# Kernel optimization log

Hardware: AMD Instinct MI355X
Metric: run time of the kernel (lower is better)

The kernel has to match this reference:

```python
import jax, jax.numpy as jnp
import numpy as np

B, S, D = 4, 1568, 1024
H = 16
HD = D // H  # 64


def setup_inputs() -> dict:
    key = jax.random.key(0)
    ks = jax.random.split(key, 9)
    scale = 0.02
    return {
        "hidden_states": jax.random.normal(ks[0], (B, S, D), dtype=jnp.float32),
        "Wq": jax.random.normal(ks[1], (D, D), dtype=jnp.float32) * scale,
        "bq": jnp.zeros((D,), dtype=jnp.float32),
        "Wk": jax.random.normal(ks[2], (D, D), dtype=jnp.float32) * scale,
        "bk": jnp.zeros((D,), dtype=jnp.float32),
        "Wv": jax.random.normal(ks[3], (D, D), dtype=jnp.float32) * scale,
        "bv": jnp.zeros((D,), dtype=jnp.float32),
        "Wp": jax.random.normal(ks[4], (D, D), dtype=jnp.float32) * scale,
        "bp": jnp.zeros((D,), dtype=jnp.float32),
    }


def reference(hidden_states, Wq, bq, Wk, bk, Wv, bv, Wp, bp):
    x = hidden_states  # [B, S, D]
    # Linear projections (torch Linear: x @ W.T + b)
    q = x @ Wq.T + bq
    k = x @ Wk.T + bk
    v = x @ Wv.T + bv
    # split heads: [B, H, S, HD]
    def heads(t):
        return t.reshape(B, S, H, HD).transpose(0, 2, 1, 3)
    q, k, v = heads(q), heads(k), heads(v)
    scale = 1.0 / jnp.sqrt(jnp.asarray(HD, dtype=q.dtype))
    scores = jnp.einsum('bhqd,bhkd->bhqk', q, k) * scale  # [B,H,S,S]
    probs = jax.nn.softmax(scores, axis=-1)
    ctx = jnp.einsum('bhqk,bhkd->bhqd', probs, v)  # [B,H,S,HD]
    ctx = ctx.transpose(0, 2, 1, 3).reshape(B, S, D)
    out = ctx @ Wp.T + bp
    return out
```

## Files before the change

kernel.cpp:

```cpp
#include <hip/hip_runtime.h>
#include <stdint.h>

#define SEQ 1568
#define SEQV 1600
#define DIM 1024
#define NB 4
#define NH 16
#define HD 64

typedef unsigned short u16;
typedef __bf16 bf16x8 __attribute__((ext_vector_type(8)));
typedef float f32x4 __attribute__((ext_vector_type(4)));

#define QSCALE 0.18033688011112042f

#define PSTR 72

__device__ __forceinline__ void load_lds16(const u16* g, u16* s) {
  __builtin_amdgcn_global_load_lds((__attribute__((address_space(1))) void*)g,
                                   (__attribute__((address_space(3))) void*)s,
                                   16, 0, 0);
}

__global__ __launch_bounds__(256) void cvt_all(
    const float* __restrict__ x,  const float* __restrict__ wq,
    const float* __restrict__ wk, const float* __restrict__ wv,
    const float* __restrict__ wp,
    u16* __restrict__ xb, u16* __restrict__ wqb, u16* __restrict__ wkb,
    u16* __restrict__ wvb, u16* __restrict__ wpb) {
  int i = blockIdx.x * 256 + threadIdx.x;
  const float* src; u16* dst; int off;
  if (i < 1605632)      { src = x;  dst = xb;  off = i; }
  else if (i < 1867776) { src = wq; dst = wqb; off = i - 1605632; }
  else if (i < 2129920) { src = wk; dst = wkb; off = i - 1867776; }
  else if (i < 2392064) { src = wv; dst = wvb; off = i - 2129920; }
  else                  { src = wp; dst = wpb; off = i - 2392064; }
  float4 v = ((const float4*)src)[off];
  union { unsigned long long u; __bf16 h[4]; } o;
  o.h[0] = (__bf16)v.x; o.h[1] = (__bf16)v.y;
  o.h[2] = (__bf16)v.z; o.h[3] = (__bf16)v.w;
  ((unsigned long long*)dst)[off] = o.u;
}

__global__ __launch_bounds__(256) void gemm_qkv(
    const u16* __restrict__ xb,
    const u16* __restrict__ wq, const u16* __restrict__ wk, const u16* __restrict__ wv,
    const float* __restrict__ bq, const float* __restrict__ bk, const float* __restrict__ bv,
    u16* __restrict__ qo, u16* __restrict__ ko, u16* __restrict__ vto) {
  const int z = blockIdx.z;
  const u16* W = (z == 0) ? wq : (z == 1) ? wk : wv;
  const float* bias = (z == 0) ? bq : (z == 1) ? bk : bv;

  __shared__ __align__(16) u16 sA[128 * 32];
  __shared__ __align__(16) u16 sB[128 * 32];

  const int tid = threadIdx.x;
  const int wave = tid >> 6;
  const int lane = tid & 63;
  const int l15 = lane & 15;
  const int quad = lane >> 4;
  const int bi = blockIdx.y / 13;
  const int st = blockIdx.y % 13;
  const int bn = blockIdx.x * 128;
  const int wm = (wave >> 1) * 64;
  const int wn = (wave & 1) * 64;

  const int sr = lane >> 2;
  const int sc = (lane & 3) * 8;
  const int r0 = wave * 32;

  f32x4 acc[4][4] = {};

  for (int k0 = 0; k0 < DIM; k0 += 32) {
    __syncthreads();
    {
      int sr1 = st * 128 + r0 + sr;       if (sr1 >= SEQ) sr1 = SEQ - 1;
      int sr2 = st * 128 + r0 + 16 + sr;  if (sr2 >= SEQ) sr2 = SEQ - 1;
      load_lds16(xb + (size_t)(bi * SEQ + sr1) * DIM + k0 + sc, &sA[r0 * 32]);
      load_lds16(xb + (size_t)(bi * SEQ + sr2) * DIM + k0 + sc, &sA[(r0 + 16) * 32]);
      const u16* gB = W + (size_t)(bn + r0 + sr) * DIM + k0 + sc;
      load_lds16(gB, &sB[r0 * 32]);
      load_lds16(gB + 16 * DIM, &sB[(r0 + 16) * 32]);
    }
    __syncthreads();

    bf16x8 a[4], b[4];
#pragma unroll
    for (int mt = 0; mt < 4; mt++)
      a[mt] = *(const bf16x8*)&sA[(wm + mt * 16 + l15) * 32 + quad * 8];
#pragma unroll
    for (int nt = 0; nt < 4; nt++)
      b[nt] = *(const bf16x8*)&sB[(wn + nt * 16 + l15) * 32 + quad * 8];
#pragma unroll
    for (int mt = 0; mt < 4; mt++)
#pragma unroll
      for (int nt = 0; nt < 4; nt++)
        acc[mt][nt] = __builtin_amdgcn_mfma_f32_16x16x32_bf16(a[mt], b[nt], acc[mt][nt], 0, 0, 0);
  }

#pragma unroll
  for (int nt = 0; nt < 4; nt++) {
    const int n = bn + wn + nt * 16 + l15;
    const float bia = bias[n];
    const int h = n >> 6, d = n & 63;
#pragma unroll
    for (int mt = 0; mt < 4; mt++) {
      const int sbase = st * 128 + wm + mt * 16 + quad * 4;
#pragma unroll
      for (int r = 0; r < 4; r++) {
        const int s = sbase + r;
        if (s < SEQ) {
          float val = acc[mt][nt][r] + bia;
          if (z == 0) val *= QSCALE;
          const __bf16 o = (__bf16)val;
          if (z == 0)
            *(__bf16*)&qo[(((size_t)(bi * NH + h)) * SEQ + s) * HD + d] = o;
          else if (z == 1)
            *(__bf16*)&ko[(((size_t)(bi * NH + h)) * SEQ + s) * HD + d] = o;
          else
            *(__bf16*)&vto[(((size_t)(bi * NH + h)) * HD + d) * SEQV + s] = o;
        }
      }
    }
  }
}

__global__ __launch_bounds__(256, 4) void attn(
    const u16* __restrict__ q, const u16* __restrict__ k,
    const u16* __restrict__ vt, u16* __restrict__ ctx) {
  const int bh = blockIdx.y;
  const int qt = blockIdx.x;
  const int tid = threadIdx.x;
  const int wave = tid >> 6, lane = tid & 63, l15 = lane & 15, quad = lane >> 4;

  __shared__ __align__(16) u16 sK[64 * 64];
  __shared__ __align__(16) u16 sV[64 * 64];
  __shared__ __align__(16) u16 sP[4][32 * PSTR];

  const u16* qh = q + (size_t)bh * (SEQ * HD);
  const u16* kh = k + (size_t)bh * (SEQ * HD);
  const u16* vh = vt + (size_t)bh * (HD * SEQV);

  bf16x8 aq[2][2];
#pragma unroll
  for (int mt = 0; mt < 2; mt++) {
    int qrow = qt * 128 + wave * 32 + mt * 16 + l15;
    int qr = qrow < SEQ ? qrow : SEQ - 1;
    aq[mt][0] = *(const bf16x8*)&qh[(size_t)qr * HD + quad * 8];
    aq[mt][1] = *(const bf16x8*)&qh[(size_t)qr * HD + 32 + quad * 8];
  }

  f32x4 o[2][4] = {};
  float lrow[2][4] = {};

  const int jrow = lane >> 3;
  const int cg = (lane & 7) ^ jrow;
  u16* sPw = sP[wave];
  const int j7 = l15 & 7;

  for (int j0 = 0; j0 < 1536; j0 += 64) {
    __syncthreads();
    load_lds16(&kh[(size_t)(j0 + wave * 16 + jrow) * HD + cg * 8], &sK[(wave * 16) * 64]);
    load_lds16(&kh[(size_t)(j0 + wave * 16 + 8 + jrow) * HD + cg * 8], &sK[(wave * 16 + 8) * 64]);
    load_lds16(&vh[(size_t)(wave * 16 + jrow) * SEQV + j0 + cg * 8], &sV[(wave * 16) * 64]);
    load_lds16(&vh[(size_t)(wave * 16 + 8 + jrow) * SEQV + j0 + cg * 8], &sV[(wave * 16 + 8) * 64]);
    __syncthreads();

#pragma unroll
    for (int mt = 0; mt < 2; mt++) {
      f32x4 s[4];
#pragma unroll
      for (int jt = 0; jt < 4; jt++) {
        const int j = jt * 16 + l15;
        bf16x8 b0 = *(const bf16x8*)&sK[j * 64 + ((quad ^ j7) * 8)];
        bf16x8 b1 = *(const bf16x8*)&sK[j * 64 + (((4 + quad) ^ j7) * 8)];
        f32x4 acc = {};
        acc = __builtin_amdgcn_mfma_f32_16x16x32_bf16(aq[mt][0], b0, acc, 0, 0, 0);
        acc = __builtin_amdgcn_mfma_f32_16x16x32_bf16(aq[mt][1], b1, acc, 0, 0, 0);
        s[jt] = acc;
      }
#pragma unroll
      for (int jt = 0; jt < 4; jt++)
#pragma unroll
        for (int r = 0; r < 4; r++) {
          float p = __builtin_exp2f(s[jt][r]);
          lrow[mt][r] += p;
          *(__bf16*)&sPw[(mt * 16 + quad * 4 + r) * PSTR + jt * 16 + l15] = (__bf16)p;
        }
    }

    asm volatile("s_waitcnt lgkmcnt(0)" ::: "memory");

#pragma unroll
    for (int kc = 0; kc < 2; kc++) {
      bf16x8 ap0 = *(const bf16x8*)&sPw[l15 * PSTR + kc * 32 + quad * 8];
      bf16x8 ap1 = *(const bf16x8*)&sPw[(16 + l15) * PSTR + kc * 32 + quad * 8];
#pragma unroll
      for (int dt = 0; dt < 4; dt++) {
        const int d7 = l15 & 7;
        bf16x8 bv = *(const bf16x8*)&sV[(dt * 16 + l15) * 64 + (((kc * 4 + quad) ^ d7) * 8)];
        o[0][dt] = __builtin_amdgcn_mfma_f32_16x16x32_bf16(ap0, bv, o[0][dt], 0, 0, 0);
        o[1][dt] = __builtin_amdgcn_mfma_f32_16x16x32_bf16(ap1, bv, o[1][dt], 0, 0, 0);
      }
    }
  }

  {
    const int j0 = 1536;
    __syncthreads();
    if (wave < 2) {
      load_lds16(&kh[(size_t)(j0 + wave * 16 + jrow) * HD + cg * 8], &sK[(wave * 16) * 64]);
      load_lds16(&kh[(size_t)(j0 + wave * 16 + 8 + jrow) * HD + cg * 8], &sK[(wave * 16 + 8) * 64]);
    }
    load_lds16(&vh[(size_t)(wave * 16 + jrow) * SEQV + j0 + cg * 8], &sV[(wave * 16) * 64]);
    load_lds16(&vh[(size_t)(wave * 16 + 8 + jrow) * SEQV + j0 + cg * 8], &sV[(wave * 16 + 8) * 64]);
    __syncthreads();

#pragma unroll
    for (int mt = 0; mt < 2; mt++) {
      f32x4 s[2];
#pragma unroll
      for (int jt = 0; jt < 2; jt++) {
        const int j = jt * 16 + l15;
        bf16x8 b0 = *(const bf16x8*)&sK[j * 64 + ((quad ^ j7) * 8)];
        bf16x8 b1 = *(const bf16x8*)&sK[j * 64 + (((4 + quad) ^ j7) * 8)];
        f32x4 acc = {};
        acc = __builtin_amdgcn_mfma_f32_16x16x32_bf16(aq[mt][0], b0, acc, 0, 0, 0);
        acc = __builtin_amdgcn_mfma_f32_16x16x32_bf16(aq[mt][1], b1, acc, 0, 0, 0);
        s[jt] = acc;
      }
#pragma unroll
      for (int jt = 0; jt < 2; jt++)
#pragma unroll
        for (int r = 0; r < 4; r++) {
          float p = __builtin_exp2f(s[jt][r]);
          lrow[mt][r] += p;
          *(__bf16*)&sPw[(mt * 16 + quad * 4 + r) * PSTR + jt * 16 + l15] = (__bf16)p;
        }
    }

    asm volatile("s_waitcnt lgkmcnt(0)" ::: "memory");

    {
      bf16x8 ap0 = *(const bf16x8*)&sPw[l15 * PSTR + quad * 8];
      bf16x8 ap1 = *(const bf16x8*)&sPw[(16 + l15) * PSTR + quad * 8];
#pragma unroll
      for (int dt = 0; dt < 4; dt++) {
        const int d7 = l15 & 7;
        bf16x8 bv = *(const bf16x8*)&sV[(dt * 16 + l15) * 64 + ((quad ^ d7) * 8)];
        o[0][dt] = __builtin_amdgcn_mfma_f32_16x16x32_bf16(ap0, bv, o[0][dt], 0, 0, 0);
        o[1][dt] = __builtin_amdgcn_mfma_f32_16x16x32_bf16(ap1, bv, o[1][dt], 0, 0, 0);
      }
    }
  }

  const int bi = bh >> 4, h = bh & 15;
#pragma unroll
  for (int mt = 0; mt < 2; mt++) {
#pragma unroll
    for (int r = 0; r < 4; r++) {
      float l = lrow[mt][r];
#pragma unroll
      for (int off = 8; off >= 1; off >>= 1) l += __shfl_xor(l, off, 16);
      const int srow = qt * 128 + wave * 32 + mt * 16 + quad * 4 + r;
      if (srow < SEQ) {
        const float inv = 1.0f / l;
#pragma unroll
        for (int dt = 0; dt < 4; dt++)
          *(__bf16*)&ctx[((size_t)(bi * SEQ + srow)) * DIM + h * HD + dt * 16 + l15] =
              (__bf16)(o[mt][dt][r] * inv);
      }
    }
  }
}

__global__ __launch_bounds__(256) void gemm_out(
    const u16* __restrict__ ctx, const u16* __restrict__ wp,
    const float* __restrict__ bp, float* __restrict__ out) {
  __shared__ __align__(16) u16 sA[128 * 32];
  __shared__ __align__(16) u16 sB[128 * 32];

  const int tid = threadIdx.x;
  const int wave = tid >> 6;
  const int lane = tid & 63;
  const int l15 = lane & 15;
  const int quad = lane >> 4;
  const int bm = blockIdx.y * 128;
  const int bn = blockIdx.x * 128;
  const int wm = (wave >> 1) * 64;
  const int wn = (wave & 1) * 64;
  const int sr = lane >> 2;
  const int sc = (lane & 3) * 8;
  const int r0 = wave * 32;

  f32x4 acc[4][4] = {};

  for (int k0 = 0; k0 < DIM; k0 += 32) {
    __syncthreads();
    {
      const u16* gA = ctx + (size_t)(bm + r0 + sr) * DIM + k0 + sc;
      load_lds16(gA, &sA[r0 * 32]);
      load_lds16(gA + 16 * DIM, &sA[(r0 + 16) * 32]);
      const u16* gB = wp + (size_t)(bn + r0 + sr) * DIM + k0 + sc;
      load_lds16(gB, &sB[r0 * 32]);
      load_lds16(gB + 16 * DIM, &sB[(r0 + 16) * 32]);
    }
    __syncthreads();

    bf16x8 a[4], b[4];
#pragma unroll
    for (int mt = 0; mt < 4; mt++)
      a[mt] = *(const bf16x8*)&sA[(wm + mt * 16 + l15) * 32 + quad * 8];
#pragma unroll
    for (int nt = 0; nt < 4; nt++)
      b[nt] = *(const bf16x8*)&sB[(wn + nt * 16 + l15) * 32 + quad * 8];
#pragma unroll
    for (int mt = 0; mt < 4; mt++)
#pragma unroll
      for (int nt = 0; nt < 4; nt++)
        acc[mt][nt] = __builtin_amdgcn_mfma_f32_16x16x32_bf16(a[mt], b[nt], acc[mt][nt], 0, 0, 0);
  }

#pragma unroll
  for (int nt = 0; nt < 4; nt++) {
    const int n = bn + wn + nt * 16 + l15;
    const float bia = bp[n];
#pragma unroll
    for (int mt = 0; mt < 4; mt++) {
      const int mbase = bm + wm + mt * 16 + quad * 4;
#pragma unroll
      for (int r = 0; r < 4; r++)
        out[(size_t)(mbase + r) * DIM + n] = acc[mt][nt][r] + bia;
    }
  }
}

extern "C" void kernel_launch(void* const* d_in, const int* in_sizes, int n_in,
                              void* d_out, int out_size, void* d_ws, size_t ws_size,
                              hipStream_t stream) {
  const float* x  = (const float*)d_in[0];
  const float* Wq = (const float*)d_in[1];
  const float* bq = (const float*)d_in[2];
  const float* Wk = (const float*)d_in[3];
  const float* bk = (const float*)d_in[4];
  const float* Wv = (const float*)d_in[5];
  const float* bv = (const float*)d_in[6];
  const float* Wp = (const float*)d_in[7];
  const float* bp = (const float*)d_in[8];
  float* out = (float*)d_out;

  char* ws = (char*)d_ws;
  u16* xb   = (u16*)(ws + 0);
  u16* wqb  = (u16*)(ws + 12845056);
  u16* wkb  = (u16*)(ws + 14942208);
  u16* wvb  = (u16*)(ws + 17039360);
  u16* wpb  = (u16*)(ws + 19136512);
  u16* qb   = (u16*)(ws + 21233664);
  u16* kb   = (u16*)(ws + 34078720);
  u16* vtb  = (u16*)(ws + 46923776);
  u16* ctxb = (u16*)(ws + 60030976);

  cvt_all<<<10368, 256, 0, stream>>>(x, Wq, Wk, Wv, Wp, xb, wqb, wkb, wvb, wpb);
  gemm_qkv<<<dim3(8, 52, 3), 256, 0, stream>>>(xb, wqb, wkb, wvb, bq, bk, bv, qb, kb, vtb);
  attn<<<dim3(13, 64), 256, 0, stream>>>(qb, kb, vtb, ctxb);
  gemm_out<<<dim3(8, 49), 256, 0, stream>>>(ctxb, wpb, bp, out);
}
```

Measured before the change: 301.2 us.

## Double-buffer LDS in QKV and output GEMMs and remap block order

Both projection GEMMs now use two LDS buffers so the global-to-LDS load of the next K slice is issued before the MFMA work on the current slice. This halves the barriers per K step and overlaps load latency with compute. Block indices are also remapped so consecutive blocks share the same weight column tile, aiming for better L2 reuse. The cost is doubled LDS use per block, which may lower occupancy.

Measured after the change: 315.3 us. 1.05x slower.

```diff
diff --git a/kernel.cpp b/kernel.cpp
--- a/kernel.cpp
+++ b/kernel.cpp
@@ -42,26 +42,57 @@
   ((unsigned long long*)dst)[off] = o.u;
 }
 
+__device__ __forceinline__ void stage4(const u16* gA1, const u16* gA2,
+                                       const u16* gB1, const u16* gB2, int kk,
+                                       u16* sAc, u16* sBc, int r0) {
+  load_lds16(gA1 + kk, sAc + r0 * 32);
+  load_lds16(gA2 + kk, sAc + (r0 + 16) * 32);
+  load_lds16(gB1 + kk, sBc + r0 * 32);
+  load_lds16(gB2 + kk, sBc + (r0 + 16) * 32);
+}
+
+__device__ __forceinline__ void mfma_tile_128(const u16* sAc, const u16* sBc,
+                                              int wm, int wn, int l15, int quad,
+                                              f32x4 acc[4][4]) {
+  bf16x8 a[4], b[4];
+#pragma unroll
+  for (int mt = 0; mt < 4; mt++)
+    a[mt] = *(const bf16x8*)&sAc[(wm + mt * 16 + l15) * 32 + quad * 8];
+#pragma unroll
+  for (int nt = 0; nt < 4; nt++)
+    b[nt] = *(const bf16x8*)&sBc[(wn + nt * 16 + l15) * 32 + quad * 8];
+#pragma unroll
+  for (int mt = 0; mt < 4; mt++)
+#pragma unroll
+    for (int nt = 0; nt < 4; nt++)
+      acc[mt][nt] = __builtin_amdgcn_mfma_f32_16x16x32_bf16(a[mt], b[nt], acc[mt][nt], 0, 0, 0);
+}
+
 __global__ __launch_bounds__(256) void gemm_qkv(
     const u16* __restrict__ xb,
     const u16* __restrict__ wq, const u16* __restrict__ wk, const u16* __restrict__ wv,
     const float* __restrict__ bq, const float* __restrict__ bk, const float* __restrict__ bv,
     u16* __restrict__ qo, u16* __restrict__ ko, u16* __restrict__ vto) {
-  const int z = blockIdx.z;
+  const int bid = blockIdx.x + (blockIdx.y << 3) + blockIdx.z * 416;
+  const int logical = (bid & 7) * 156 + (bid >> 3);
+  const int byz = logical >> 3;
+  const int by  = byz % 52;
+  const int z   = byz / 52;
+  const int bi  = by / 13;
+  const int st  = by % 13;
+  const int bn  = (logical & 7) * 128;
+
   const u16* W = (z == 0) ? wq : (z == 1) ? wk : wv;
   const float* bias = (z == 0) ? bq : (z == 1) ? bk : bv;
 
-  __shared__ __align__(16) u16 sA[128 * 32];
-  __shared__ __align__(16) u16 sB[128 * 32];
+  __shared__ __align__(16) u16 sA[2][128 * 32];
+  __shared__ __align__(16) u16 sB[2][128 * 32];
 
   const int tid = threadIdx.x;
   const int wave = tid >> 6;
   const int lane = tid & 63;
   const int l15 = lane & 15;
   const int quad = lane >> 4;
-  const int bi = blockIdx.y / 13;
-  const int st = blockIdx.y % 13;
-  const int bn = blockIdx.x * 128;
   const int wm = (wave >> 1) * 64;
   const int wn = (wave & 1) * 64;
 
@@ -69,33 +100,29 @@
   const int sc = (lane & 3) * 8;
   const int r0 = wave * 32;
 
+  int sr1 = st * 128 + r0 + sr;       if (sr1 >= SEQ) sr1 = SEQ - 1;
+  int sr2 = st * 128 + r0 + 16 + sr;  if (sr2 >= SEQ) sr2 = SEQ - 1;
+  const u16* gA1 = xb + (size_t)(bi * SEQ + sr1) * DIM + sc;
+  const u16* gA2 = xb + (size_t)(bi * SEQ + sr2) * DIM + sc;
+  const u16* gB1 = W + (size_t)(bn + r0 + sr) * DIM + sc;
+  const u16* gB2 = gB1 + 16 * DIM;
+
   f32x4 acc[4][4] = {};
 
-  for (int k0 = 0; k0 < DIM; k0 += 32) {
-    __syncthreads();
-    {
-      int sr1 = st * 128 + r0 + sr;       if (sr1 >= SEQ) sr1 = SEQ - 1;
-      int sr2 = st * 128 + r0 + 16 + sr;  if (sr2 >= SEQ) sr2 = SEQ - 1;
-      load_lds16(xb + (size_t)(bi * SEQ + sr1) * DIM + k0 + sc, &sA[r0 * 32]);
-      load_lds16(xb + (size_t)(bi * SEQ + sr2) * DIM + k0 + sc, &sA[(r0 + 16) * 32]);
-      const u16* gB = W + (size_t)(bn + r0 + sr) * DIM + k0 + sc;
-      load_lds16(gB, &sB[r0 * 32]);
-      load_lds16(gB + 16 * DIM, &sB[(r0 + 16) * 32]);
-    }
-    __syncthreads();
-
-    bf16x8 a[4], b[4];
-#pragma unroll
-    for (int mt = 0; mt < 4; mt++)
-      a[mt] = *(const bf16x8*)&sA[(wm + mt * 16 + l15) * 32 + quad * 8];
-#pragma unroll
-    for (int nt = 0; nt < 4; nt++)
-      b[nt] = *(const bf16x8*)&sB[(wn + nt * 16 + l15) * 32 + quad * 8];
-#pragma unroll
-    for (int mt = 0; mt < 4; mt++)
-#pragma unroll
-      for (int nt = 0; nt < 4; nt++)
-        acc[mt][nt] = __builtin_amdgcn_mfma_f32_16x16x32_bf16(a[mt], b[nt], acc[mt][nt], 0, 0, 0);
+  u16* sA0 = &sA[0][0]; u16* sA1 = &sA[1][0];
+  u16* sB0 = &sB[0][0]; u16* sB1 = &sB[1][0];
+
+  stage4(gA1, gA2, gB1, gB2, 0, sA0, sB0, r0);
+  __syncthreads();
+
+#pragma unroll 1
+  for (int k0 = 0; k0 < DIM; k0 += 64) {
+    stage4(gA1, gA2, gB1, gB2, k0 + 32, sA1, sB1, r0);
+    mfma_tile_128(sA0, sB0, wm, wn, l15, quad, acc);
+    __syncthreads();
+    if (k0 + 64 < DIM) stage4(gA1, gA2, gB1, gB2, k0 + 64, sA0, sB0, r0);
+    mfma_tile_128(sA1, sB1, wm, wn, l15, quad, acc);
+    __syncthreads();
   }
 
 #pragma unroll
@@ -277,48 +304,46 @@
 __global__ __launch_bounds__(256) void gemm_out(
     const u16* __restrict__ ctx, const u16* __restrict__ wp,
     const float* __restrict__ bp, float* __restrict__ out) {
-  __shared__ __align__(16) u16 sA[128 * 32];
-  __shared__ __align__(16) u16 sB[128 * 32];
+  __shared__ __align__(16) u16 sA[2][128 * 32];
+  __shared__ __align__(16) u16 sB[2][128 * 32];
+
+  const int bid = blockIdx.x + (blockIdx.y << 3);
+  const int logical = (bid & 7) * 49 + (bid >> 3);
+  const int bn = (logical & 7) * 128;
+  const int bm = (logical >> 3) * 128;
 
   const int tid = threadIdx.x;
   const int wave = tid >> 6;
   const int lane = tid & 63;
   const int l15 = lane & 15;
   const int quad = lane >> 4;
-  const int bm = blockIdx.y * 128;
-  const int bn = blockIdx.x * 128;
   const int wm = (wave >> 1) * 64;
   const int wn = (wave & 1) * 64;
   const int sr = lane >> 2;
   const int sc = (lane & 3) * 8;
   const int r0 = wave * 32;
 
+  const u16* gA1 = ctx + (size_t)(bm + r0 + sr) * DIM + sc;
+  const u16* gA2 = gA1 + 16 * DIM;
+  const u16* gB1 = wp + (size_t)(bn + r0 + sr) * DIM + sc;
+  const u16* gB2 = gB1 + 16 * DIM;
+
   f32x4 acc[4][4] = {};
 
-  for (int k0 = 0; k0 < DIM; k0 += 32) {
-    __syncthreads();
-    {
-      const u16* gA = ctx + (size_t)(bm + r0 + sr) * DIM + k0 + sc;
-      load_lds16(gA, &sA[r0 * 32]);
-      load_lds16(gA + 16 * DIM, &sA[(r0 + 16) * 32]);
-      const u16* gB = wp + (size_t)(bn + r0 + sr) * DIM + k0 + sc;
-      load_lds16(gB, &sB[r0 * 32]);
-      load_lds16(gB + 16 * DIM, &sB[(r0 + 16) * 32]);
-    }
-    __syncthreads();
-
-    bf16x8 a[4], b[4];
-#pragma unroll
-    for (int mt = 0; mt < 4; mt++)
-      a[mt] = *(const bf16x8*)&sA[(wm + mt * 16 + l15) * 32 + quad * 8];
-#pragma unroll
-    for (int nt = 0; nt < 4; nt++)
-      b[nt] = *(const bf16x8*)&sB[(wn + nt * 16 + l15) * 32 + quad * 8];
-#pragma unroll
-    for (int mt = 0; mt < 4; mt++)
-#pragma unroll
-      for (int nt = 0; nt < 4; nt++)
-        acc[mt][nt] = __builtin_amdgcn_mfma_f32_16x16x32_bf16(a[mt], b[nt], acc[mt][nt], 0, 0, 0);
+  u16* sA0 = &sA[0][0]; u16* sA1 = &sA[1][0];
+  u16* sB0 = &sB[0][0]; u16* sB1 = &sB[1][0];
+
+  stage4(gA1, gA2, gB1, gB2, 0, sA0, sB0, r0);
+  __syncthreads();
+
+#pragma unroll 1
+  for (int k0 = 0; k0 < DIM; k0 += 64) {
+    stage4(gA1, gA2, gB1, gB2, k0 + 32, sA1, sB1, r0);
+    mfma_tile_128(sA0, sB0, wm, wn, l15, quad, acc);
+    __syncthreads();
+    if (k0 + 64 < DIM) stage4(gA1, gA2, gB1, gB2, k0 + 64, sA0, sB0, r0);
+    mfma_tile_128(sA1, sB1, wm, wn, l15, quad, acc);
+    __syncthreads();
   }
 
 #pragma unroll
```

## Restructure QKV GEMM with fused weight stack, wider tiles, double-buffered LDS and swizzle

Applied to the files above, without the earlier changes.

The QKV projection now runs as one GEMM over the three stacked bf16 weight matrices, relying on the converted Wq/Wk/Wv sitting back to back in the workspace. It uses 128x256 block tiles with a 64x128 tile per wave, and double-buffers the LDS loads so the next k-slice is fetched while MFMAs run on the current one. It adds an XOR swizzle on LDS columns to cut bank conflicts, and a block-index remap meant to improve L2 locality. The larger accumulator (32 f32x4 per thread) raises register pressure under the occupancy hint of 2 blocks per CU.

Measured after the change: 313.0 us. +3.9%, slower.

```diff
diff --git a/kernel.cpp b/kernel.cpp
--- a/kernel.cpp
+++ b/kernel.cpp
@@ -42,67 +42,87 @@
   ((unsigned long long*)dst)[off] = o.u;
 }
 
-__global__ __launch_bounds__(256) void gemm_qkv(
-    const u16* __restrict__ xb,
-    const u16* __restrict__ wq, const u16* __restrict__ wk, const u16* __restrict__ wv,
+__global__ __launch_bounds__(256, 2) void gemm_qkv(
+    const u16* __restrict__ xb, const u16* __restrict__ wstk,
     const float* __restrict__ bq, const float* __restrict__ bk, const float* __restrict__ bv,
     u16* __restrict__ qo, u16* __restrict__ ko, u16* __restrict__ vto) {
-  const int z = blockIdx.z;
-  const u16* W = (z == 0) ? wq : (z == 1) ? wk : wv;
-  const float* bias = (z == 0) ? bq : (z == 1) ? bk : bv;
-
-  __shared__ __align__(16) u16 sA[128 * 32];
-  __shared__ __align__(16) u16 sB[128 * 32];
+  const int bid = blockIdx.x;
+  const int logical = (bid & 7) * 78 + (bid >> 3);
+  const int ntile = logical % 12;
+  const int mtile = logical / 12;
+  const int bi = mtile / 13;
+  const int st = mtile % 13;
+  const int bn = ntile * 256;
+
+  __shared__ __align__(16) u16 sA[2][128 * 32];
+  __shared__ __align__(16) u16 sB[2][256 * 32];
 
   const int tid = threadIdx.x;
-  const int wave = tid >> 6;
-  const int lane = tid & 63;
-  const int l15 = lane & 15;
-  const int quad = lane >> 4;
-  const int bi = blockIdx.y / 13;
-  const int st = blockIdx.y % 13;
-  const int bn = blockIdx.x * 128;
+  const int wave = tid >> 6, lane = tid & 63, l15 = lane & 15, quad = lane >> 4;
   const int wm = (wave >> 1) * 64;
-  const int wn = (wave & 1) * 64;
+  const int wn = (wave & 1) * 128;
 
   const int sr = lane >> 2;
-  const int sc = (lane & 3) * 8;
-  const int r0 = wave * 32;
-
-  f32x4 acc[4][4] = {};
-
-  for (int k0 = 0; k0 < DIM; k0 += 32) {
-    __syncthreads();
-    {
-      int sr1 = st * 128 + r0 + sr;       if (sr1 >= SEQ) sr1 = SEQ - 1;
-      int sr2 = st * 128 + r0 + 16 + sr;  if (sr2 >= SEQ) sr2 = SEQ - 1;
-      load_lds16(xb + (size_t)(bi * SEQ + sr1) * DIM + k0 + sc, &sA[r0 * 32]);
-      load_lds16(xb + (size_t)(bi * SEQ + sr2) * DIM + k0 + sc, &sA[(r0 + 16) * 32]);
-      const u16* gB = W + (size_t)(bn + r0 + sr) * DIM + k0 + sc;
-      load_lds16(gB, &sB[r0 * 32]);
-      load_lds16(gB + 16 * DIM, &sB[(r0 + 16) * 32]);
-    }
-    __syncthreads();
-
-    bf16x8 a[4], b[4];
+  const int scs = (((lane & 3) ^ ((lane >> 3) & 3)) << 3);
+
+  int ra1 = st * 128 + wave * 32 + sr;       if (ra1 >= SEQ) ra1 = SEQ - 1;
+  int ra2 = st * 128 + wave * 32 + 16 + sr;  if (ra2 >= SEQ) ra2 = SEQ - 1;
+  const u16* gA1 = xb + (size_t)(bi * SEQ + ra1) * DIM + scs;
+  const u16* gA2 = xb + (size_t)(bi * SEQ + ra2) * DIM + scs;
+  const u16* gB  = wstk + (size_t)(bn + wave * 64 + sr) * DIM + scs;
+
+  const int dA = wave * 32 * 32;
+  const int dB = wave * 64 * 32;
+
+  f32x4 acc[4][8] = {};
+
+  u16* sA0 = &sA[0][0]; u16* sA1 = &sA[1][0];
+  u16* sB0 = &sB[0][0]; u16* sB1 = &sB[1][0];
+
+  auto stage = [&](int kk, u16* sAc, u16* sBc) {
+    load_lds16(gA1 + kk, sAc + dA);
+    load_lds16(gA2 + kk, sAc + dA + 16 * 32);
+#pragma unroll
+    for (int i = 0; i < 4; i++)
+      load_lds16(gB + (size_t)i * 16 * DIM + kk, sBc + dB + i * 16 * 32);
+  };
+
+  const int rsw = (l15 >> 1) & 3;
+
+  auto mstep = [&](const u16* sAc, const u16* sBc) {
+    bf16x8 a[4], b[8];
 #pragma unroll
     for (int mt = 0; mt < 4; mt++)
-      a[mt] = *(const bf16x8*)&sA[(wm + mt * 16 + l15) * 32 + quad * 8];
-#pragma unroll
-    for (int nt = 0; nt < 4; nt++)
-      b[nt] = *(const bf16x8*)&sB[(wn + nt * 16 + l15) * 32 + quad * 8];
+      a[mt] = *(const bf16x8*)&sAc[(wm + mt * 16 + l15) * 32 + ((quad ^ rsw) << 3)];
+#pragma unroll
+    for (int nt = 0; nt < 8; nt++)
+      b[nt] = *(const bf16x8*)&sBc[(wn + nt * 16 + l15) * 32 + ((quad ^ rsw) << 3)];
 #pragma unroll
     for (int mt = 0; mt < 4; mt++)
 #pragma unroll
-      for (int nt = 0; nt < 4; nt++)
+      for (int nt = 0; nt < 8; nt++)
         acc[mt][nt] = __builtin_amdgcn_mfma_f32_16x16x32_bf16(a[mt], b[nt], acc[mt][nt], 0, 0, 0);
-  }
-
-#pragma unroll
-  for (int nt = 0; nt < 4; nt++) {
+  };
+
+  stage(0, sA0, sB0);
+  __syncthreads();
+
+#pragma unroll 1
+  for (int k0 = 0; k0 < DIM; k0 += 64) {
+    stage(k0 + 32, sA1, sB1);
+    mstep(sA0, sB0);
+    __syncthreads();
+    if (k0 + 64 < DIM) stage(k0 + 64, sA0, sB0);
+    mstep(sA1, sB1);
+    __syncthreads();
+  }
+
+#pragma unroll
+  for (int nt = 0; nt < 8; nt++) {
     const int n = bn + wn + nt * 16 + l15;
-    const float bia = bias[n];
-    const int h = n >> 6, d = n & 63;
+    const int z = n >> 10, n1 = n & 1023;
+    const float bia = (z == 0 ? bq : z == 1 ? bk : bv)[n1];
+    const int h = n1 >> 6, d = n1 & 63;
 #pragma unroll
     for (int mt = 0; mt < 4; mt++) {
       const int sbase = st * 128 + wm + mt * 16 + quad * 4;
@@ -361,7 +381,7 @@
   u16* ctxb = (u16*)(ws + 60030976);
 
   cvt_all<<<10368, 256, 0, stream>>>(x, Wq, Wk, Wv, Wp, xb, wqb, wkb, wvb, wpb);
-  gemm_qkv<<<dim3(8, 52, 3), 256, 0, stream>>>(xb, wqb, wkb, wvb, bq, bk, bv, qb, kb, vtb);
+  gemm_qkv<<<624, 256, 0, stream>>>(xb, wqb, bq, bk, bv, qb, kb, vtb);
   attn<<<dim3(13, 64), 256, 0, stream>>>(qb, kb, vtb, ctxb);
   gemm_out<<<dim3(8, 49), 256, 0, stream>>>(ctxb, wpb, bp, out);
 }
```

## Triple-buffer QKV GEMM LDS loads with swizzle and XCD-aware block remap

Applied to the files above, without the earlier changes.

Replaces the single-buffered QKV projection GEMM main loop with a three-stage LDS ring. Direct-to-LDS global loads for future k-tiles are issued while MFMAs run on the current tile, synchronised with explicit vmcnt waits and barriers. It also XOR-swizzles the LDS column layout to reduce bank conflicts, and remaps block IDs so neighbouring tiles land on the same XCD for L2 reuse. The cost is three times the LDS footprint, which may lower occupancy, plus hand-counted waitcnt logic that is fragile.

After: 295.6 us. About the same (-1.9%).

```diff
diff --git a/kernel.cpp b/kernel.cpp
--- a/kernel.cpp
+++ b/kernel.cpp
@@ -21,6 +21,11 @@
                                    (__attribute__((address_space(3))) void*)s,
                                    16, 0, 0);
 }
+
+#define WAIT_VM(N) asm volatile("s_waitcnt vmcnt(" #N ")" ::: "memory")
+#define LGKM0()    asm volatile("s_waitcnt lgkmcnt(0)" ::: "memory")
+#define BAR()      do { __builtin_amdgcn_s_barrier(); \
+                        __builtin_amdgcn_sched_barrier(0); } while (0)
 
 __global__ __launch_bounds__(256) void cvt_all(
     const float* __restrict__ x,  const float* __restrict__ wq,
@@ -47,56 +52,90 @@
     const u16* __restrict__ wq, const u16* __restrict__ wk, const u16* __restrict__ wv,
     const float* __restrict__ bq, const float* __restrict__ bk, const float* __restrict__ bv,
     u16* __restrict__ qo, u16* __restrict__ ko, u16* __restrict__ vto) {
-  const int z = blockIdx.z;
+  const int bid = blockIdx.x + (blockIdx.y << 3) + blockIdx.z * 416;
+  const int logical = (bid & 7) * 156 + (bid >> 3);
+  const int byz = logical >> 3;
+  const int by  = byz % 52;
+  const int z   = byz / 52;
+  const int bi  = by / 13;
+  const int st  = by % 13;
+  const int bn  = (logical & 7) * 128;
+
   const u16* W = (z == 0) ? wq : (z == 1) ? wk : wv;
   const float* bias = (z == 0) ? bq : (z == 1) ? bk : bv;
 
-  __shared__ __align__(16) u16 sA[128 * 32];
-  __shared__ __align__(16) u16 sB[128 * 32];
+  __shared__ __align__(16) u16 sA[3][128 * 32];
+  __shared__ __align__(16) u16 sB[3][128 * 32];
 
   const int tid = threadIdx.x;
   const int wave = tid >> 6;
   const int lane = tid & 63;
   const int l15 = lane & 15;
   const int quad = lane >> 4;
-  const int bi = blockIdx.y / 13;
-  const int st = blockIdx.y % 13;
-  const int bn = blockIdx.x * 128;
   const int wm = (wave >> 1) * 64;
   const int wn = (wave & 1) * 64;
 
-  const int sr = lane >> 2;
-  const int sc = (lane & 3) * 8;
+  const int sr  = lane >> 2;
+  const int scs = (((lane & 3) ^ ((lane >> 3) & 3)) << 3);
   const int r0 = wave * 32;
 
+  int ra1 = st * 128 + r0 + sr;       if (ra1 >= SEQ) ra1 = SEQ - 1;
+  int ra2 = st * 128 + r0 + 16 + sr;  if (ra2 >= SEQ) ra2 = SEQ - 1;
+  const u16* gA1 = xb + (size_t)(bi * SEQ + ra1) * DIM + scs;
+  const u16* gA2 = xb + (size_t)(bi * SEQ + ra2) * DIM + scs;
+  const u16* gB1 = W + (size_t)(bn + r0 + sr) * DIM + scs;
+  const u16* gB2 = gB1 + 16 * DIM;
+
   f32x4 acc[4][4] = {};
-
-  for (int k0 = 0; k0 < DIM; k0 += 32) {
-    __syncthreads();
-    {
-      int sr1 = st * 128 + r0 + sr;       if (sr1 >= SEQ) sr1 = SEQ - 1;
-      int sr2 = st * 128 + r0 + 16 + sr;  if (sr2 >= SEQ) sr2 = SEQ - 1;
-      load_lds16(xb + (size_t)(bi * SEQ + sr1) * DIM + k0 + sc, &sA[r0 * 32]);
-      load_lds16(xb + (size_t)(bi * SEQ + sr2) * DIM + k0 + sc, &sA[(r0 + 16) * 32]);
-      const u16* gB = W + (size_t)(bn + r0 + sr) * DIM + k0 + sc;
-      load_lds16(gB, &sB[r0 * 32]);
-      load_lds16(gB + 16 * DIM, &sB[(r0 + 16) * 32]);
-    }
-    __syncthreads();
-
+  const int rsw = (l15 >> 1) & 3;
+
+  auto stage = [&](int kk, u16* sAc, u16* sBc) {
+    load_lds16(gA1 + kk, sAc + r0 * 32);
+    load_lds16(gA2 + kk, sAc + (r0 + 16) * 32);
+    load_lds16(gB1 + kk, sBc + r0 * 32);
+    load_lds16(gB2 + kk, sBc + (r0 + 16) * 32);
+  };
+
+  auto mstep = [&](const u16* sAc, const u16* sBc) {
     bf16x8 a[4], b[4];
 #pragma unroll
     for (int mt = 0; mt < 4; mt++)
-      a[mt] = *(const bf16x8*)&sA[(wm + mt * 16 + l15) * 32 + quad * 8];
+      a[mt] = *(const bf16x8*)&sAc[(wm + mt * 16 + l15) * 32 + ((quad ^ rsw) << 3)];
 #pragma unroll
     for (int nt = 0; nt < 4; nt++)
-      b[nt] = *(const bf16x8*)&sB[(wn + nt * 16 + l15) * 32 + quad * 8];
+      b[nt] = *(const bf16x8*)&sBc[(wn + nt * 16 + l15) * 32 + ((quad ^ rsw) << 3)];
 #pragma unroll
     for (int mt = 0; mt < 4; mt++)
 #pragma unroll
       for (int nt = 0; nt < 4; nt++)
         acc[mt][nt] = __builtin_amdgcn_mfma_f32_16x16x32_bf16(a[mt], b[nt], acc[mt][nt], 0, 0, 0);
-  }
+  };
+
+  stage(0,  &sA[0][0], &sB[0][0]);
+  stage(32, &sA[1][0], &sB[1][0]);
+  stage(64, &sA[2][0], &sB[2][0]);
+
+#pragma unroll 1
+  for (int t = 0; t < 30; t += 3) {
+    WAIT_VM(8); BAR();
+    mstep(&sA[0][0], &sB[0][0]);
+    LGKM0(); BAR();
+    stage((t + 3) * 32, &sA[0][0], &sB[0][0]);
+
+    WAIT_VM(8); BAR();
+    mstep(&sA[1][0], &sB[1][0]);
+    LGKM0(); BAR();
+    stage((t + 4) * 32, &sA[1][0], &sB[1][0]);
+
+    WAIT_VM(8); BAR();
+    mstep(&sA[2][0], &sB[2][0]);
+    LGKM0(); BAR();
+    if (t + 5 < 32) stage((t + 5) * 32, &sA[2][0], &sB[2][0]);
+  }
+  WAIT_VM(4); BAR();
+  mstep(&sA[0][0], &sB[0][0]);
+  WAIT_VM(0); BAR();
+  mstep(&sA[1][0], &sB[1][0]);
 
 #pragma unroll
   for (int nt = 0; nt < 4; nt++) {
```
